# Kernel optimization log

Hardware: AMD Instinct MI355X
Metric: run time of the kernel (lower is better)

Reference implementation:

```python
import jax, jax.numpy as jnp
import numpy as np

NH, NKVH, HD = 32, 8, 128
SCALE = 0.08838834764831845  # 1/sqrt(128)
SEQ, CTX = 1024, 3072       # new chunk tokens, cached context tokens
NSLOTS = 8192               # e.g. 512 blocks * block_size 16, slot-flattened


def setup_inputs() -> dict:
    key = jax.random.key(0)
    ks = jax.random.split(key, 5)
    q = jax.random.normal(ks[0], (SEQ, NH * HD), dtype=jnp.float32)
    k = jax.random.normal(ks[1], (SEQ, NKVH * HD), dtype=jnp.float32)
    v = jax.random.normal(ks[2], (SEQ, NKVH * HD), dtype=jnp.float32)
    k_cache = jax.random.normal(ks[3], (NSLOTS, NKVH, HD), dtype=jnp.float32)
    v_cache = jax.random.normal(ks[4], (NSLOTS, NKVH, HD), dtype=jnp.float32)
    # new chunk is stored right after the context region
    slot_mapping = jnp.arange(SEQ, dtype=jnp.int32) + CTX
    context_slots = jnp.arange(CTX, dtype=jnp.int32)
    return {"q": q, "k": k, "v": v, "k_cache": k_cache, "v_cache": v_cache,
            "slot_mapping": slot_mapping, "context_slots": context_slots}


def reference(q, k, v, k_cache, v_cache, slot_mapping, context_slots):
    seq = q.shape[0]
    ctx = context_slots.shape[0]
    qh = q.reshape(seq, NH, HD)
    kh = k.reshape(seq, NKVH, HD)
    vh = v.reshape(seq, NKVH, HD)

    # store_kv_cache: scatter new chunk k/v into paged cache slots
    kc = k_cache.at[slot_mapping].set(kh)
    vc = v_cache.at[slot_mapping].set(vh)

    # gather cached context, then chunked-prefill attention over [ctx | chunk]
    k_all = jnp.concatenate([kc[context_slots], kh], axis=0)  # [L, nkvh, hd]
    v_all = jnp.concatenate([vc[context_slots], vh], axis=0)  # [L, nkvh, hd]
    L = ctx + seq

    group = NH // NKVH
    qg = qh.reshape(seq, NKVH, group, HD) * SCALE
    scores = jnp.einsum('qkgd,lkd->kgql', qg, k_all)  # [nkvh, group, seq, L]

    # full visibility of cached context, causal within the new chunk
    mask = jnp.arange(L)[None, :] <= (ctx + jnp.arange(seq))[:, None]  # [seq, L]
    scores = jnp.where(mask[None, None], scores, jnp.finfo(scores.dtype).min)
    p = jax.nn.softmax(scores, axis=-1)

    o = jnp.einsum('kgql,lkd->qkgd', p, v_all)  # [seq, nkvh, group, hd]
    return o.reshape(seq, NH * HD)
```

## Files before the change

### kernel.cpp

```cpp
#include <hip/hip_runtime.h>

#define NH 32
#define NKVH 8
#define HD 128
#define GRP 4
#define SCALE 0.08838834764831845f
#define LOG2E 1.4426950408889634f
#define PSTR 72
#define THR 8.0f

typedef __attribute__((ext_vector_type(8))) __bf16 bf16x8;
typedef __attribute__((ext_vector_type(4))) float f32x4;
typedef __attribute__((ext_vector_type(8))) unsigned short ushort8;

union U8 { ushort8 u; unsigned int d[4]; bf16x8 h; };

__device__ inline unsigned int cvt_pk_bf16(float lo, float hi) {
  unsigned int r;
  asm("v_cvt_pk_bf16_f32 %0, %1, %2" : "=v"(r) : "v"(lo), "v"(hi));
  return r;
}

__device__ inline float fast_exp2(float x) {
#if __has_builtin(__builtin_amdgcn_exp2f)
  return __builtin_amdgcn_exp2f(x);
#else
  return exp2f(x);
#endif
}

__device__ inline float dpp_max16(float x) {
  x = fmaxf(x, __int_as_float(__builtin_amdgcn_mov_dpp(__float_as_int(x), 0xB1, 0xF, 0xF, true)));
  x = fmaxf(x, __int_as_float(__builtin_amdgcn_mov_dpp(__float_as_int(x), 0x4E, 0xF, 0xF, true)));
  x = fmaxf(x, __int_as_float(__builtin_amdgcn_mov_dpp(__float_as_int(x), 0x141, 0xF, 0xF, true)));
  x = fmaxf(x, __int_as_float(__builtin_amdgcn_mov_dpp(__float_as_int(x), 0x140, 0xF, 0xF, true)));
  return x;
}
__device__ inline float dpp_sum16(float x) {
  x += __int_as_float(__builtin_amdgcn_mov_dpp(__float_as_int(x), 0xB1, 0xF, 0xF, true));
  x += __int_as_float(__builtin_amdgcn_mov_dpp(__float_as_int(x), 0x4E, 0xF, 0xF, true));
  x += __int_as_float(__builtin_amdgcn_mov_dpp(__float_as_int(x), 0x141, 0xF, 0xF, true));
  x += __int_as_float(__builtin_amdgcn_mov_dpp(__float_as_int(x), 0x140, 0xF, 0xF, true));
  return x;
}

__device__ inline void load_lds16(const unsigned short* g, unsigned short* l) {
  __builtin_amdgcn_global_load_lds((const __attribute__((address_space(1))) unsigned int*)g,
                                   (__attribute__((address_space(3))) unsigned int*)l, 16, 0, 0);
}

__global__ __launch_bounds__(256) void prepass_kernel(
    const float* __restrict__ k, const float* __restrict__ v,
    const float* __restrict__ kc, const float* __restrict__ vc,
    const int* __restrict__ slots,
    unsigned short* __restrict__ Kws, unsigned short* __restrict__ Vws,
    int ctx, int L, int kblocks)
{
  if (blockIdx.x < (unsigned)kblocks) {
    const int idx = blockIdx.x * 256 + threadIdx.x;
    const int L8  = L * 8;
    const int kvh = idx / L8;
    const int r2  = idx - kvh * L8;
    const int l   = r2 >> 3;
    const int c16 = idx & 7;
    const float* src = (l < ctx)
        ? kc + ((size_t)slots[l] * NKVH + kvh) * HD + c16 * 16
        : k + (size_t)(l - ctx) * (NKVH * HD) + kvh * HD + c16 * 16;
    float4 f[4];
#pragma unroll
    for (int i = 0; i < 4; ++i) f[i] = ((const float4*)src)[i];
    unsigned short* tile = Kws + (size_t)kvh * L * HD + (size_t)(l >> 6) * 8192;
    const int r = l & 63;
    const int c0 = (2 * c16) ^ (r & 7);
    const int c1 = (2 * c16 + 1) ^ (r & 7);
    U8 w0, w1;
    w0.d[0] = cvt_pk_bf16(f[0].x, f[0].y); w0.d[1] = cvt_pk_bf16(f[0].z, f[0].w);
    w0.d[2] = cvt_pk_bf16(f[1].x, f[1].y); w0.d[3] = cvt_pk_bf16(f[1].z, f[1].w);
    w1.d[0] = cvt_pk_bf16(f[2].x, f[2].y); w1.d[1] = cvt_pk_bf16(f[2].z, f[2].w);
    w1.d[2] = cvt_pk_bf16(f[3].x, f[3].y); w1.d[3] = cvt_pk_bf16(f[3].z, f[3].w);
    *(ushort8*)&tile[r * 128 + c0 * 8] = w0.u;
    *(ushort8*)&tile[r * 128 + c1 * 8] = w1.u;
  } else {
    const int idx = (blockIdx.x - kblocks) * 256 + threadIdx.x;
    const int d   = idx & 127;
    const int t2  = idx >> 7;
    const int L16 = L >> 4;
    const int kvh = t2 / L16;
    const int lc  = t2 - kvh * L16;
    const int l0  = lc * 16;
    const int lB  = l0 & ~63;
    const int pc2 = (l0 >> 4) & 3;
    float vals[16];
#pragma unroll
    for (int j = 0; j < 16; ++j) {
      const int l = lB + ((j & 3) << 4) + pc2 * 4 + (j >> 2);
      const float* sp = (l < ctx)
          ? vc + ((size_t)slots[l] * NKVH + kvh) * HD + d
          : v + (size_t)(l - ctx) * (NKVH * HD) + kvh * HD + d;
      vals[j] = *sp;
    }
    U8 w0, w1;
#pragma unroll
    for (int i = 0; i < 4; ++i) {
      w0.d[i] = cvt_pk_bf16(vals[2 * i],     vals[2 * i + 1]);
      w1.d[i] = cvt_pk_bf16(vals[8 + 2 * i], vals[9 + 2 * i]);
    }
    unsigned short* tile = Vws + (size_t)kvh * L * HD + (size_t)(l0 >> 6) * 8192;
    const int lt  = l0 & 63;
    const int cl0 = lt >> 3;
    *(ushort8*)&tile[d * 64 + ((cl0 ^ (d & 7)) * 8)] = w0.u;
    *(ushort8*)&tile[d * 64 + (((cl0 + 1) ^ (d & 7)) * 8)] = w1.u;
  }
}

__global__ __launch_bounds__(256, 2) void attn_kernel(
    const float* __restrict__ q,
    const unsigned short* __restrict__ Kws, const unsigned short* __restrict__ Vws,
    float* __restrict__ out, int ctx, int L)
{
  __shared__ __align__(16) unsigned short Ks[2][8192];
  __shared__ __align__(16) unsigned short VTs[2][8192];
  __shared__ __align__(16) unsigned short Ps[4 * 16 * PSTR];

  const int bx   = blockIdx.x;
  const int kvh  = bx & 7;
  const int g    = (bx >> 3) & 3;
  const int qb   = bx >> 5;
  const int q0   = qb * 64;
  const int head = kvh * GRP + g;

  const int tid  = threadIdx.x;
  const int wave = tid >> 6;
  const int lane = tid & 63;
  const int col  = lane & 15;
  const int quad = lane >> 4;

  bf16x8 qf[4];
  {
    const float s2 = SCALE * LOG2E;
    const float* qp = q + (size_t)(q0 + wave * 16 + col) * (NH * HD) + head * HD;
#pragma unroll
    for (int kt = 0; kt < 4; ++kt) {
      const float4 a = *(const float4*)(qp + kt * 32 + quad * 8);
      const float4 b = *(const float4*)(qp + kt * 32 + quad * 8 + 4);
      U8 w;
      w.d[0] = cvt_pk_bf16(a.x * s2, a.y * s2);
      w.d[1] = cvt_pk_bf16(a.z * s2, a.w * s2);
      w.d[2] = cvt_pk_bf16(b.x * s2, b.y * s2);
      w.d[3] = cvt_pk_bf16(b.z * s2, b.w * s2);
      qf[kt] = w.h;
    }
  }

  f32x4 accO[8];
#pragma unroll
  for (int i = 0; i < 8; ++i) accO[i] = (f32x4){0.f, 0.f, 0.f, 0.f};
  float mrow = -1e30f;
  float lrow[4] = {0.f, 0.f, 0.f, 0.f};

  const int rowbase = q0 + wave * 16 + quad * 4;
  const size_t kvbase = (size_t)kvh * L * HD;
  const int n_tiles = (ctx + q0 + 64) >> 6;

  auto dma_tile = [&](int t, int b) {
    const unsigned short* kg = Kws + kvbase + (size_t)t * 8192;
    const unsigned short* vg = Vws + kvbase + (size_t)t * 8192;
#pragma unroll
    for (int j = 0; j < 4; ++j) {
      const int ch = wave * 4 + j;
      load_lds16(kg + ch * 512 + lane * 8, &Ks[b][ch * 512]);
      load_lds16(vg + ch * 512 + lane * 8, &VTs[b][ch * 512]);
    }
  };

  dma_tile(0, 0);

  for (int it = 0; it < n_tiles; ++it) {
    __syncthreads();

    if (it + 1 < n_tiles) dma_tile(it + 1, (it + 1) & 1);

    const unsigned short* Kb = Ks[it & 1];
    const unsigned short* Vb = VTs[it & 1];
    const int kb = it << 6;

    f32x4 S[4];
#pragma unroll
    for (int nt = 0; nt < 4; ++nt) S[nt] = (f32x4){0.f, 0.f, 0.f, 0.f};
#pragma unroll
    for (int kt = 0; kt < 4; ++kt)
#pragma unroll
      for (int nt = 0; nt < 4; ++nt) {
        const int row = nt * 16 + col;
        const bf16x8 kf = *(const bf16x8*)&Kb[row * 128 + (((kt * 4 + quad) ^ (row & 7)) << 3)];
        S[nt] = __builtin_amdgcn_mfma_f32_16x16x32_bf16(qf[kt], kf, S[nt], 0, 0, 0);
      }

    bf16x8 vf[8][2];
#pragma unroll
    for (int nt = 0; nt < 8; ++nt) {
      const int d = nt * 16 + col;
#pragma unroll
      for (int kt = 0; kt < 2; ++kt)
        vf[nt][kt] = *(const bf16x8*)&Vb[d * 64 + (((kt * 4 + quad) ^ (d & 7)) << 3)];
    }

    if (kb + 63 > ctx + q0 + wave * 16) {
#pragma unroll
      for (int r = 0; r < 4; ++r) {
        const int bound = ctx + rowbase + r;
#pragma unroll
        for (int nt = 0; nt < 4; ++nt) {
          const int l = kb + nt * 16 + col;
          if (l > bound) S[nt][r] = -1e30f;
        }
      }
    }

    float M = fmaxf(fmaxf(S[0][0], S[0][1]), fmaxf(S[0][2], S[0][3]));
    M = fmaxf(M, fmaxf(fmaxf(S[1][0], S[1][1]), fmaxf(S[1][2], S[1][3])));
    M = fmaxf(M, fmaxf(fmaxf(S[2][0], S[2][1]), fmaxf(S[2][2], S[2][3])));
    M = fmaxf(M, fmaxf(fmaxf(S[3][0], S[3][1]), fmaxf(S[3][2], S[3][3])));
    M = dpp_max16(M);
    if (!__all(M - mrow <= THR)) {
      const float mnew = fmaxf(mrow, M);
      const float a = fast_exp2(mrow - mnew);
      mrow = mnew;
#pragma unroll
      for (int r = 0; r < 4; ++r) lrow[r] *= a;
#pragma unroll
      for (int dd = 0; dd < 8; ++dd)
#pragma unroll
        for (int r = 0; r < 4; ++r) accO[dd][r] *= a;
    }
#pragma unroll
    for (int nt = 0; nt < 4; ++nt)
#pragma unroll
      for (int r = 0; r < 4; ++r) {
        const float p = fast_exp2(S[nt][r] - mrow);
        S[nt][r] = p;
        lrow[r] += p;
      }

    unsigned short* pw = &Ps[wave * 16 * PSTR];
#pragma unroll
    for (int r = 0; r < 4; ++r) {
      const unsigned long long lo = cvt_pk_bf16(S[0][r], S[1][r]);
      const unsigned long long hi = cvt_pk_bf16(S[2][r], S[3][r]);
      *(unsigned long long*)&pw[(quad * 4 + r) * PSTR + col * 4] = lo | (hi << 32);
    }
    asm volatile("s_waitcnt lgkmcnt(0)" ::: "memory");

    const bf16x8 pf0 = *(const bf16x8*)&pw[col * PSTR + quad * 8];
    const bf16x8 pf1 = *(const bf16x8*)&pw[col * PSTR + 32 + quad * 8];

#pragma unroll
    for (int nt = 0; nt < 8; ++nt) {
      accO[nt] = __builtin_amdgcn_mfma_f32_16x16x32_bf16(pf0, vf[nt][0], accO[nt], 0, 0, 0);
      accO[nt] = __builtin_amdgcn_mfma_f32_16x16x32_bf16(pf1, vf[nt][1], accO[nt], 0, 0, 0);
    }
  }

  float inv[4];
#pragma unroll
  for (int r = 0; r < 4; ++r) {
    lrow[r] = dpp_sum16(lrow[r]);
    inv[r] = 1.0f / lrow[r];
  }
  float* op = out + head * HD;
#pragma unroll
  for (int r = 0; r < 4; ++r) {
    float* orow = op + (size_t)(rowbase + r) * (NH * HD);
#pragma unroll
    for (int nt = 0; nt < 8; ++nt)
      orow[nt * 16 + col] = accO[nt][r] * inv[r];
  }
}

extern "C" void kernel_launch(void* const* d_in, const int* in_sizes, int n_in,
                              void* d_out, int out_size, void* d_ws, size_t ws_size,
                              hipStream_t stream) {
  const float* q  = (const float*)d_in[0];
  const float* k  = (const float*)d_in[1];
  const float* v  = (const float*)d_in[2];
  const float* kc = (const float*)d_in[3];
  const float* vc = (const float*)d_in[4];
  const int* ctx_slots = (const int*)d_in[6];
  float* out = (float*)d_out;

  const int seq = in_sizes[0] / (NH * HD);
  const int ctx = in_sizes[6];
  const int L   = ctx + seq;

  unsigned short* Kws = (unsigned short*)d_ws;
  unsigned short* Vws = Kws + (size_t)NKVH * L * HD;

  const int kthreads = NKVH * L * (HD / 16);
  const int vthreads = NKVH * (L / 16) * HD;
  const int kblocks  = kthreads / 256;
  const int vblocks  = vthreads / 256;
  prepass_kernel<<<kblocks + vblocks, 256, 0, stream>>>(k, v, kc, vc, ctx_slots,
                                                        Kws, Vws, ctx, L, kblocks);

  const int nblocks = (seq / 64) * GRP * NKVH;
  attn_kernel<<<nblocks, 256, 0, stream>>>(q, Kws, Vws, out, ctx, L);
}
```

Measured before the change: 222.2 us.

## Rework attention into 32x32 MFMA with GQA head sharing and split-KV merge

The attention kernel now runs 512-thread blocks, one per KV head and 32-query tile. The four query heads of a GQA group share each K/V tile loaded into LDS, and the block's two wave-groups each take half of the KV tiles. The split halves are merged at the end through an LDS log-sum-exp combine. The math switches to 32x32x16 bf16 MFMA with S^T, so P stays in registers via cross-lane shuffles instead of an LDS round trip, and the V prepass layout is changed to match. This is meant to cut redundant K/V traffic and LDS P staging. In exchange it uses one block per CU, a larger register footprint, and a final merge step.

```diff
diff --git a/kernel.cpp b/kernel.cpp
--- a/kernel.cpp
+++ b/kernel.cpp
@@ -6,11 +6,11 @@
 #define GRP 4
 #define SCALE 0.08838834764831845f
 #define LOG2E 1.4426950408889634f
-#define PSTR 72
 #define THR 8.0f
 
 typedef __attribute__((ext_vector_type(8))) __bf16 bf16x8;
 typedef __attribute__((ext_vector_type(4))) float f32x4;
+typedef __attribute__((ext_vector_type(16))) float f32x16;
 typedef __attribute__((ext_vector_type(8))) unsigned short ushort8;
 
 union U8 { ushort8 u; unsigned int d[4]; bf16x8 h; };
@@ -27,21 +27,6 @@
 #else
   return exp2f(x);
 #endif
-}
-
-__device__ inline float dpp_max16(float x) {
-  x = fmaxf(x, __int_as_float(__builtin_amdgcn_mov_dpp(__float_as_int(x), 0xB1, 0xF, 0xF, true)));
-  x = fmaxf(x, __int_as_float(__builtin_amdgcn_mov_dpp(__float_as_int(x), 0x4E, 0xF, 0xF, true)));
-  x = fmaxf(x, __int_as_float(__builtin_amdgcn_mov_dpp(__float_as_int(x), 0x141, 0xF, 0xF, true)));
-  x = fmaxf(x, __int_as_float(__builtin_amdgcn_mov_dpp(__float_as_int(x), 0x140, 0xF, 0xF, true)));
-  return x;
-}
-__device__ inline float dpp_sum16(float x) {
-  x += __int_as_float(__builtin_amdgcn_mov_dpp(__float_as_int(x), 0xB1, 0xF, 0xF, true));
-  x += __int_as_float(__builtin_amdgcn_mov_dpp(__float_as_int(x), 0x4E, 0xF, 0xF, true));
-  x += __int_as_float(__builtin_amdgcn_mov_dpp(__float_as_int(x), 0x141, 0xF, 0xF, true));
-  x += __int_as_float(__builtin_amdgcn_mov_dpp(__float_as_int(x), 0x140, 0xF, 0xF, true));
-  return x;
 }
 
 __device__ inline void load_lds16(const unsigned short* g, unsigned short* l) {
@@ -88,16 +73,14 @@
     const int kvh = t2 / L16;
     const int lc  = t2 - kvh * L16;
     const int l0  = lc * 16;
-    const int lB  = l0 & ~63;
-    const int pc2 = (l0 >> 4) & 3;
     float vals[16];
 #pragma unroll
-    for (int j = 0; j < 16; ++j) {
-      const int l = lB + ((j & 3) << 4) + pc2 * 4 + (j >> 2);
+    for (int i = 0; i < 16; ++i) {
+      const int l = l0 + i;
       const float* sp = (l < ctx)
           ? vc + ((size_t)slots[l] * NKVH + kvh) * HD + d
           : v + (size_t)(l - ctx) * (NKVH * HD) + kvh * HD + d;
-      vals[j] = *sp;
+      vals[i] = *sp;
     }
     U8 w0, w1;
 #pragma unroll
@@ -113,167 +96,246 @@
   }
 }
 
-__global__ __launch_bounds__(256, 2) void attn_kernel(
+__global__ __launch_bounds__(512, 1) void attn_kernel(
     const float* __restrict__ q,
     const unsigned short* __restrict__ Kws, const unsigned short* __restrict__ Vws,
     float* __restrict__ out, int ctx, int L)
 {
-  __shared__ __align__(16) unsigned short Ks[2][8192];
-  __shared__ __align__(16) unsigned short VTs[2][8192];
-  __shared__ __align__(16) unsigned short Ps[4 * 16 * PSTR];
-
-  const int bx   = blockIdx.x;
-  const int kvh  = bx & 7;
-  const int g    = (bx >> 3) & 3;
-  const int qb   = bx >> 5;
-  const int q0   = qb * 64;
-  const int head = kvh * GRP + g;
+  __shared__ __align__(16) unsigned short lds[65536];
+
+  const int bx  = blockIdx.x;
+  const int kvh = bx & 7;
+  const int qb  = bx >> 3;
+  const int q0  = qb * 32;
 
   const int tid  = threadIdx.x;
   const int wave = tid >> 6;
   const int lane = tid & 63;
-  const int col  = lane & 15;
-  const int quad = lane >> 4;
-
-  bf16x8 qf[4];
+  const int l31  = lane & 31;
+  const int hi   = lane >> 5;
+  const int g2   = wave >> 2;
+  const int g    = wave & 3;
+  const int head = kvh * GRP + g;
+  const int swz  = (hi ^ (lane & 7)) << 3;
+
+  bf16x8 qf[8];
   {
     const float s2 = SCALE * LOG2E;
-    const float* qp = q + (size_t)(q0 + wave * 16 + col) * (NH * HD) + head * HD;
-#pragma unroll
-    for (int kt = 0; kt < 4; ++kt) {
-      const float4 a = *(const float4*)(qp + kt * 32 + quad * 8);
-      const float4 b = *(const float4*)(qp + kt * 32 + quad * 8 + 4);
+    const float* qp = q + (size_t)(q0 + l31) * (NH * HD) + head * HD + hi * 8;
+#pragma unroll
+    for (int ks = 0; ks < 8; ++ks) {
+      const float4 a = *(const float4*)(qp + ks * 16);
+      const float4 b = *(const float4*)(qp + ks * 16 + 4);
       U8 w;
       w.d[0] = cvt_pk_bf16(a.x * s2, a.y * s2);
       w.d[1] = cvt_pk_bf16(a.z * s2, a.w * s2);
       w.d[2] = cvt_pk_bf16(b.x * s2, b.y * s2);
       w.d[3] = cvt_pk_bf16(b.z * s2, b.w * s2);
-      qf[kt] = w.h;
-    }
-  }
-
-  f32x4 accO[8];
-#pragma unroll
-  for (int i = 0; i < 8; ++i) accO[i] = (f32x4){0.f, 0.f, 0.f, 0.f};
-  float mrow = -1e30f;
-  float lrow[4] = {0.f, 0.f, 0.f, 0.f};
-
-  const int rowbase = q0 + wave * 16 + quad * 4;
+      qf[ks] = w.h;
+    }
+  }
+
+  f32x16 accO[4];
+#pragma unroll
+  for (int i = 0; i < 4; ++i)
+#pragma unroll
+    for (int r = 0; r < 16; ++r) accO[i][r] = 0.f;
+  float m = -1e30f;
+  float lrow = 0.f;
+
   const size_t kvbase = (size_t)kvh * L * HD;
-  const int n_tiles = (ctx + q0 + 64) >> 6;
-
-  auto dma_tile = [&](int t, int b) {
-    const unsigned short* kg = Kws + kvbase + (size_t)t * 8192;
-    const unsigned short* vg = Vws + kvbase + (size_t)t * 8192;
+  const unsigned short* Kg = Kws + kvbase;
+  const unsigned short* Vg = Vws + kvbase;
+
+  const int nt = (ctx + q0 + 95) >> 6;
+  const int n0 = (nt + 1) >> 1;
+  const int n1 = nt - n0;
+  const int tbase = g2 ? n0 : 0;
+  const int tcnt  = g2 ? n1 : n0;
+
+  auto dma_tile = [&](int tg, int b) {
+    unsigned short* Kt = &lds[(g2 * 2 + b) * 16384];
+    unsigned short* Vt = Kt + 8192;
+    const unsigned short* kg = Kg + (size_t)tg * 8192;
+    const unsigned short* vg = Vg + (size_t)tg * 8192;
 #pragma unroll
     for (int j = 0; j < 4; ++j) {
-      const int ch = wave * 4 + j;
-      load_lds16(kg + ch * 512 + lane * 8, &Ks[b][ch * 512]);
-      load_lds16(vg + ch * 512 + lane * 8, &VTs[b][ch * 512]);
+      const int ch = g * 4 + j;
+      load_lds16(kg + ch * 512 + lane * 8, &Kt[ch * 512]);
+      load_lds16(vg + ch * 512 + lane * 8, &Vt[ch * 512]);
     }
   };
 
-  dma_tile(0, 0);
-
-  for (int it = 0; it < n_tiles; ++it) {
+  dma_tile(tbase, 0);
+
+  for (int j = 0; j < n0; ++j) {
     __syncthreads();
-
-    if (it + 1 < n_tiles) dma_tile(it + 1, (it + 1) & 1);
-
-    const unsigned short* Kb = Ks[it & 1];
-    const unsigned short* Vb = VTs[it & 1];
-    const int kb = it << 6;
-
-    f32x4 S[4];
-#pragma unroll
-    for (int nt = 0; nt < 4; ++nt) S[nt] = (f32x4){0.f, 0.f, 0.f, 0.f};
-#pragma unroll
-    for (int kt = 0; kt < 4; ++kt)
-#pragma unroll
-      for (int nt = 0; nt < 4; ++nt) {
-        const int row = nt * 16 + col;
-        const bf16x8 kf = *(const bf16x8*)&Kb[row * 128 + (((kt * 4 + quad) ^ (row & 7)) << 3)];
-        S[nt] = __builtin_amdgcn_mfma_f32_16x16x32_bf16(qf[kt], kf, S[nt], 0, 0, 0);
-      }
-
-    bf16x8 vf[8][2];
-#pragma unroll
-    for (int nt = 0; nt < 8; ++nt) {
-      const int d = nt * 16 + col;
-#pragma unroll
-      for (int kt = 0; kt < 2; ++kt)
-        vf[nt][kt] = *(const bf16x8*)&Vb[d * 64 + (((kt * 4 + quad) ^ (d & 7)) << 3)];
-    }
-
-    if (kb + 63 > ctx + q0 + wave * 16) {
-#pragma unroll
-      for (int r = 0; r < 4; ++r) {
-        const int bound = ctx + rowbase + r;
-#pragma unroll
-        for (int nt = 0; nt < 4; ++nt) {
-          const int l = kb + nt * 16 + col;
-          if (l > bound) S[nt][r] = -1e30f;
+    if (j + 1 < tcnt) dma_tile(tbase + j + 1, (j + 1) & 1);
+    if (j < tcnt) {
+      const int tg = tbase + j;
+      const unsigned short* Kt = &lds[(g2 * 2 + (j & 1)) * 16384];
+      const unsigned short* Vt = Kt + 8192;
+
+      f32x16 S0, S1;
+#pragma unroll
+      for (int r = 0; r < 16; ++r) { S0[r] = 0.f; S1[r] = 0.f; }
+      const int bk0 = l31 * 128 + swz;
+      const int bk1 = bk0 + 4096;
+      __builtin_amdgcn_s_setprio(1);
+#pragma unroll
+      for (int ks = 0; ks < 8; ++ks) {
+        const bf16x8 k0 = *(const bf16x8*)&Kt[bk0 ^ (ks << 4)];
+        const bf16x8 k1 = *(const bf16x8*)&Kt[bk1 ^ (ks << 4)];
+        S0 = __builtin_amdgcn_mfma_f32_32x32x16_bf16(k0, qf[ks], S0, 0, 0, 0);
+        S1 = __builtin_amdgcn_mfma_f32_32x32x16_bf16(k1, qf[ks], S1, 0, 0, 0);
+      }
+      __builtin_amdgcn_s_setprio(0);
+
+      const int kb = tg << 6;
+      if (tg == nt - 1) {
+        const int bound = ctx + q0 + l31;
+#pragma unroll
+        for (int r = 0; r < 16; ++r) {
+          const int lof = (r & 3) + 8 * (r >> 2) + 4 * hi;
+          if (kb + lof > bound)      S0[r] = -1e30f;
+          if (kb + 32 + lof > bound) S1[r] = -1e30f;
         }
       }
-    }
-
-    float M = fmaxf(fmaxf(S[0][0], S[0][1]), fmaxf(S[0][2], S[0][3]));
-    M = fmaxf(M, fmaxf(fmaxf(S[1][0], S[1][1]), fmaxf(S[1][2], S[1][3])));
-    M = fmaxf(M, fmaxf(fmaxf(S[2][0], S[2][1]), fmaxf(S[2][2], S[2][3])));
-    M = fmaxf(M, fmaxf(fmaxf(S[3][0], S[3][1]), fmaxf(S[3][2], S[3][3])));
-    M = dpp_max16(M);
-    if (!__all(M - mrow <= THR)) {
-      const float mnew = fmaxf(mrow, M);
-      const float a = fast_exp2(mrow - mnew);
-      mrow = mnew;
-#pragma unroll
-      for (int r = 0; r < 4; ++r) lrow[r] *= a;
-#pragma unroll
-      for (int dd = 0; dd < 8; ++dd)
-#pragma unroll
-        for (int r = 0; r < 4; ++r) accO[dd][r] *= a;
-    }
-#pragma unroll
-    for (int nt = 0; nt < 4; ++nt)
-#pragma unroll
-      for (int r = 0; r < 4; ++r) {
-        const float p = fast_exp2(S[nt][r] - mrow);
-        S[nt][r] = p;
-        lrow[r] += p;
-      }
-
-    unsigned short* pw = &Ps[wave * 16 * PSTR];
-#pragma unroll
-    for (int r = 0; r < 4; ++r) {
-      const unsigned long long lo = cvt_pk_bf16(S[0][r], S[1][r]);
-      const unsigned long long hi = cvt_pk_bf16(S[2][r], S[3][r]);
-      *(unsigned long long*)&pw[(quad * 4 + r) * PSTR + col * 4] = lo | (hi << 32);
-    }
-    asm volatile("s_waitcnt lgkmcnt(0)" ::: "memory");
-
-    const bf16x8 pf0 = *(const bf16x8*)&pw[col * PSTR + quad * 8];
-    const bf16x8 pf1 = *(const bf16x8*)&pw[col * PSTR + 32 + quad * 8];
-
-#pragma unroll
-    for (int nt = 0; nt < 8; ++nt) {
-      accO[nt] = __builtin_amdgcn_mfma_f32_16x16x32_bf16(pf0, vf[nt][0], accO[nt], 0, 0, 0);
-      accO[nt] = __builtin_amdgcn_mfma_f32_16x16x32_bf16(pf1, vf[nt][1], accO[nt], 0, 0, 0);
-    }
-  }
-
-  float inv[4];
-#pragma unroll
-  for (int r = 0; r < 4; ++r) {
-    lrow[r] = dpp_sum16(lrow[r]);
-    inv[r] = 1.0f / lrow[r];
-  }
-  float* op = out + head * HD;
-#pragma unroll
-  for (int r = 0; r < 4; ++r) {
-    float* orow = op + (size_t)(rowbase + r) * (NH * HD);
-#pragma unroll
-    for (int nt = 0; nt < 8; ++nt)
-      orow[nt * 16 + col] = accO[nt][r] * inv[r];
+
+      float t0 = fmaxf(fmaxf(S0[0], S0[1]), fmaxf(S0[2], S0[3]));
+      float t1 = fmaxf(fmaxf(S0[4], S0[5]), fmaxf(S0[6], S0[7]));
+      float t2 = fmaxf(fmaxf(S0[8], S0[9]), fmaxf(S0[10], S0[11]));
+      float t3 = fmaxf(fmaxf(S0[12], S0[13]), fmaxf(S0[14], S0[15]));
+      float u0 = fmaxf(fmaxf(S1[0], S1[1]), fmaxf(S1[2], S1[3]));
+      float u1 = fmaxf(fmaxf(S1[4], S1[5]), fmaxf(S1[6], S1[7]));
+      float u2 = fmaxf(fmaxf(S1[8], S1[9]), fmaxf(S1[10], S1[11]));
+      float u3 = fmaxf(fmaxf(S1[12], S1[13]), fmaxf(S1[14], S1[15]));
+      float M = fmaxf(fmaxf(fmaxf(t0, t1), fmaxf(t2, t3)),
+                      fmaxf(fmaxf(u0, u1), fmaxf(u2, u3)));
+      const float Mp = fmaxf(M, __shfl_xor(M, 32));
+      if (!__all(Mp - m <= THR)) {
+        const float mnew = fmaxf(m, Mp);
+        const float a = fast_exp2(m - mnew);
+        m = mnew;
+        lrow *= a;
+#pragma unroll
+        for (int i = 0; i < 4; ++i)
+#pragma unroll
+          for (int r = 0; r < 16; ++r) accO[i][r] *= a;
+      }
+      float lr0 = 0.f, lr1 = 0.f;
+#pragma unroll
+      for (int r = 0; r < 16; ++r) {
+        S0[r] = fast_exp2(S0[r] - m);
+        S1[r] = fast_exp2(S1[r] - m);
+        lr0 += S0[r];
+        lr1 += S1[r];
+      }
+      lrow += lr0 + lr1;
+
+      bf16x8 pfr[4];
+#pragma unroll
+      for (int h2 = 0; h2 < 2; ++h2) {
+        {
+          const unsigned int A = cvt_pk_bf16(S0[h2 * 8 + 0], S0[h2 * 8 + 1]);
+          const unsigned int B = cvt_pk_bf16(S0[h2 * 8 + 2], S0[h2 * 8 + 3]);
+          const unsigned int C = cvt_pk_bf16(S0[h2 * 8 + 4], S0[h2 * 8 + 5]);
+          const unsigned int D = cvt_pk_bf16(S0[h2 * 8 + 6], S0[h2 * 8 + 7]);
+          const unsigned int y1 = hi ? A : C;
+          const unsigned int y2 = hi ? B : D;
+          const unsigned int p1 = __shfl_xor(y1, 32);
+          const unsigned int p2 = __shfl_xor(y2, 32);
+          U8 w;
+          w.d[0] = hi ? p1 : A;
+          w.d[1] = hi ? p2 : B;
+          w.d[2] = hi ? C : p1;
+          w.d[3] = hi ? D : p2;
+          pfr[h2] = w.h;
+        }
+        {
+          const unsigned int A = cvt_pk_bf16(S1[h2 * 8 + 0], S1[h2 * 8 + 1]);
+          const unsigned int B = cvt_pk_bf16(S1[h2 * 8 + 2], S1[h2 * 8 + 3]);
+          const unsigned int C = cvt_pk_bf16(S1[h2 * 8 + 4], S1[h2 * 8 + 5]);
+          const unsigned int D = cvt_pk_bf16(S1[h2 * 8 + 6], S1[h2 * 8 + 7]);
+          const unsigned int y1 = hi ? A : C;
+          const unsigned int y2 = hi ? B : D;
+          const unsigned int p1 = __shfl_xor(y1, 32);
+          const unsigned int p2 = __shfl_xor(y2, 32);
+          U8 w;
+          w.d[0] = hi ? p1 : A;
+          w.d[1] = hi ? p2 : B;
+          w.d[2] = hi ? C : p1;
+          w.d[3] = hi ? D : p2;
+          pfr[2 + h2] = w.h;
+        }
+      }
+
+      __builtin_amdgcn_s_setprio(1);
+#pragma unroll
+      for (int mdt = 0; mdt < 4; ++mdt) {
+        const int bv = mdt * 2048 + l31 * 64 + swz;
+#pragma unroll
+        for (int ks = 0; ks < 4; ++ks) {
+          const bf16x8 vf = *(const bf16x8*)&Vt[bv ^ (ks << 4)];
+          accO[mdt] = __builtin_amdgcn_mfma_f32_32x32x16_bf16(vf, pfr[ks], accO[mdt], 0, 0, 0);
+        }
+      }
+      __builtin_amdgcn_s_setprio(0);
+    }
+  }
+
+  const float lsum = lrow + __shfl_xor(lrow, 32);
+
+  __syncthreads();
+  float* Om  = (float*)lds;
+  float* Mst = Om + 4 * 32 * 132;
+  float* Lst = Mst + 128;
+  float* orow = &Om[(g * 32 + l31) * 132];
+
+  if (g2 == 1) {
+#pragma unroll
+    for (int mdt = 0; mdt < 4; ++mdt)
+#pragma unroll
+      for (int qd = 0; qd < 4; ++qd) {
+        float4 w = { accO[mdt][qd * 4 + 0], accO[mdt][qd * 4 + 1],
+                     accO[mdt][qd * 4 + 2], accO[mdt][qd * 4 + 3] };
+        *(float4*)&orow[mdt * 32 + qd * 8 + hi * 4] = w;
+      }
+    if (hi == 0) { Mst[g * 32 + l31] = m; Lst[g * 32 + l31] = lsum; }
+  }
+  __syncthreads();
+  if (g2 == 0) {
+    const float m1 = Mst[g * 32 + l31];
+    const float l1 = Lst[g * 32 + l31];
+    const float mm = fmaxf(m, m1);
+    const float a0 = fast_exp2(m - mm);
+    const float a1 = fast_exp2(m1 - mm);
+    const float inv = 1.0f / (lsum * a0 + l1 * a1);
+    const float c0 = a0 * inv, c1 = a1 * inv;
+#pragma unroll
+    for (int mdt = 0; mdt < 4; ++mdt)
+#pragma unroll
+      for (int qd = 0; qd < 4; ++qd) {
+        float4 w1 = *(float4*)&orow[mdt * 32 + qd * 8 + hi * 4];
+        float4 w;
+        w.x = accO[mdt][qd * 4 + 0] * c0 + w1.x * c1;
+        w.y = accO[mdt][qd * 4 + 1] * c0 + w1.y * c1;
+        w.z = accO[mdt][qd * 4 + 2] * c0 + w1.z * c1;
+        w.w = accO[mdt][qd * 4 + 3] * c0 + w1.w * c1;
+        *(float4*)&orow[mdt * 32 + qd * 8 + hi * 4] = w;
+      }
+  }
+  __syncthreads();
+
+  {
+    const int rh = tid >> 2;
+    const int gg = rh >> 5, qq = rh & 31;
+    const int dc = (tid & 3) * 32;
+    const float* src = &Om[(gg * 32 + qq) * 132 + dc];
+    float* dst = out + (size_t)(q0 + qq) * (NH * HD) + (kvh * GRP + gg) * HD + dc;
+#pragma unroll
+    for (int i = 0; i < 8; ++i)
+      *(float4*)(dst + i * 4) = *(const float4*)(src + i * 4);
   }
 }
 
@@ -302,6 +364,6 @@
   prepass_kernel<<<kblocks + vblocks, 256, 0, stream>>>(k, v, kc, vc, ctx_slots,
                                                         Kws, Vws, ctx, L, kblocks);
 
-  const int nblocks = (seq / 64) * GRP * NKVH;
-  attn_kernel<<<nblocks, 256, 0, stream>>>(q, Kws, Vws, out, ctx, L);
-}
+  const int nblocks = (seq / 32) * NKVH;
+  attn_kernel<<<nblocks, 512, 0, stream>>>(q, Kws, Vws, out, ctx, L);
+}
```

Result: faster. 207.5 us (-6.6%).
